# Kernel tuning notes

Measured on AMD Instinct MI355X. Metric: run time of the kernel, lower is better.

The kernel has to match this reference:

```python
import jax, jax.numpy as jnp
import numpy as np

B, C, G = 2, 256, 32
SPATIAL = (16, 16, 16)
EPS = 1e-5


def setup_inputs() -> dict:
    key = jax.random.key(0)
    ks = jax.random.split(key, 11)
    s = 1.0 / np.sqrt(C)
    x = jax.random.normal(ks[0], (B, C) + SPATIAL, dtype=jnp.float32)
    mk = lambda k: jax.random.normal(k, (C, C), dtype=jnp.float32) * s
    return {
        "x": x,
        "Wq": mk(ks[1]), "bq": jnp.zeros((C,), jnp.float32),
        "Wk": mk(ks[2]), "bk": jnp.zeros((C,), jnp.float32),
        "Wv": mk(ks[3]), "bv": jnp.zeros((C,), jnp.float32),
        "Wo": mk(ks[4]), "bo": jnp.zeros((C,), jnp.float32),
        "gamma": jnp.ones((C,), jnp.float32),
        "beta": jnp.zeros((C,), jnp.float32),
    }


def reference(x, Wq, bq, Wk, bk, Wv, bv, Wo, bo, gamma, beta):
    b, c = x.shape[0], x.shape[1]
    xf = x.reshape(b, c, -1)  # [B, C, N]

    def proj1x1(inp, W, bias):
        return jnp.einsum('oc,bcn->bon', W, inp) + bias[None, :, None]

    q = proj1x1(xf, Wq, bq)
    k = proj1x1(xf, Wk, bk)
    v = proj1x1(xf, Wv, bv)

    # qk[b, n, m] = sum_c q[b, c, n] * k[b, c, m]   (no 1/sqrt(C) scale, as in source)
    scores = jnp.einsum('bcn,bcm->bnm', q, k)
    w = jax.nn.softmax(scores, axis=-1)
    # h[b, c, n] = sum_m v[b, c, m] * w[b, n, m]
    h = jnp.einsum('bcm,bnm->bcn', v, w)
    h = proj1x1(h, Wo, bo)

    y = xf + h  # residual

    # GroupNorm over (channels-in-group, spatial)
    yg = y.reshape(b, G, c // G, -1)
    mu = jnp.mean(yg, axis=(2, 3), keepdims=True)
    var = jnp.var(yg, axis=(2, 3), keepdims=True)
    yn = ((yg - mu) * jax.lax.rsqrt(var + EPS)).reshape(b, c, -1)
    yn = yn * gamma[None, :, None] + beta[None, :, None]

    out = yn * jax.nn.sigmoid(yn)  # SiLU
    return out.reshape(x.shape)
```

## Files before the change

### kernel.cpp

```cpp
#include <hip/hip_runtime.h>
#include <hip/hip_bf16.h>

typedef _Float16 f16;
typedef __attribute__((ext_vector_type(8))) _Float16 f16x8;
typedef __attribute__((ext_vector_type(4))) float f32x4;

#define CD 256
#define ND 4096
#define GD 32
#define KS 4
#define KVB 64
#define NIT ((ND / KS) / KVB)

__device__ __forceinline__ void gl_lds16(const f16* g, f16* l) {
    __builtin_amdgcn_global_load_lds(
        (const __attribute__((address_space(1))) unsigned int*)g,
        (__attribute__((address_space(3))) unsigned int*)l,
        16, 0, 0);
}

__global__ __launch_bounds__(256)
void k_proj_qkv(const float* __restrict__ x,
                const float* __restrict__ Wq, const float* __restrict__ bq,
                const float* __restrict__ Wk, const float* __restrict__ bk,
                const float* __restrict__ Wv, const float* __restrict__ bv,
                f16* __restrict__ Qt, f16* __restrict__ Kt, f16* __restrict__ Vb)
{
    __shared__ f16 As[64][40];
    __shared__ f16 Bs[64][40];
    __shared__ f16 Ts[64][72];

    const int t  = threadIdx.x;
    const int n0 = blockIdx.x * 64;
    const int o0 = blockIdx.y * 64;
    const int p  = blockIdx.z % 3;
    const int bb = blockIdx.z / 3;

    const float* W    = (p == 0) ? Wq : (p == 1) ? Wk : Wv;
    const float* bias = (p == 0) ? bq : (p == 1) ? bk : bv;

    const int w  = t >> 6;
    const int l  = t & 63;
    const int lr = l & 15;
    const int lg = l >> 4;
    const int wo = (w >> 1) * 32;
    const int wn = (w & 1) * 32;

    const int sl = t & 63;
    const int k8 = (t >> 6) * 8;

    f32x4 acc[2][2] = {};

    for (int ck = 0; ck < CD; ck += 32) {
        __syncthreads();
        {
            const float* s = W + (size_t)(o0 + sl) * CD + ck + k8;
            f16x8 v;
#pragma unroll
            for (int u = 0; u < 8; ++u) v[u] = (f16)s[u];
            *(f16x8*)&As[sl][k8] = v;
        }
        {
            const float* s = x + ((size_t)bb * CD + ck + k8) * ND + n0 + sl;
            f16x8 v;
#pragma unroll
            for (int u = 0; u < 8; ++u) v[u] = (f16)s[(size_t)u * ND];
            *(f16x8*)&Bs[sl][k8] = v;
        }
        __syncthreads();
        f16x8 a0 = *(const f16x8*)&As[wo + lr][lg * 8];
        f16x8 a1 = *(const f16x8*)&As[wo + 16 + lr][lg * 8];
        f16x8 b0 = *(const f16x8*)&Bs[wn + lr][lg * 8];
        f16x8 b1 = *(const f16x8*)&Bs[wn + 16 + lr][lg * 8];
        acc[0][0] = __builtin_amdgcn_mfma_f32_16x16x32_f16(a0, b0, acc[0][0], 0, 0, 0);
        acc[0][1] = __builtin_amdgcn_mfma_f32_16x16x32_f16(a0, b1, acc[0][1], 0, 0, 0);
        acc[1][0] = __builtin_amdgcn_mfma_f32_16x16x32_f16(a1, b0, acc[1][0], 0, 0, 0);
        acc[1][1] = __builtin_amdgcn_mfma_f32_16x16x32_f16(a1, b1, acc[1][1], 0, 0, 0);
    }

    if (p < 2) {
        __syncthreads();
#pragma unroll
        for (int so = 0; so < 2; ++so)
#pragma unroll
            for (int r = 0; r < 4; ++r) {
                int orow  = wo + so * 16 + lg * 4 + r;
                float bv_ = bias[o0 + orow];
#pragma unroll
                for (int sn = 0; sn < 2; ++sn)
                    Ts[orow][wn + sn * 16 + lr] = (f16)(acc[so][sn][r] + bv_);
            }
        __syncthreads();
        f16* dst = (p == 0) ? Qt : Kt;
        int n  = t >> 2;
        int o8 = (t & 3) * 16;
        f16 tmp[16];
#pragma unroll
        for (int u = 0; u < 16; ++u) tmp[u] = Ts[o8 + u][n];
        f16* g = dst + ((size_t)bb * ND + n0 + n) * CD + o0 + o8;
        *(f16x8*)g       = *(f16x8*)&tmp[0];
        *(f16x8*)(g + 8) = *(f16x8*)&tmp[8];
    } else {
#pragma unroll
        for (int so = 0; so < 2; ++so)
#pragma unroll
            for (int r = 0; r < 4; ++r) {
                int orow  = wo + so * 16 + lg * 4 + r;
                float bv_ = bias[o0 + orow];
#pragma unroll
                for (int sn = 0; sn < 2; ++sn) {
                    int ncol = wn + sn * 16 + lr;
                    Vb[((size_t)bb * CD + o0 + orow) * ND + n0 + ncol] =
                        (f16)(acc[so][sn][r] + bv_);
                }
            }
    }
}

__global__ __launch_bounds__(512, 2)
void k_attn(const f16* __restrict__ Qt, const f16* __restrict__ Kt,
            const f16* __restrict__ Vb, f16* __restrict__ Op,
            float* __restrict__ ml)
{
    __shared__ f16 Ks[2][64 * 256];
    __shared__ f16 Vs[2][256 * 64];
    __shared__ f16 Ps[8][16][72];

    const int t  = threadIdx.x;
    const int w  = t >> 6;
    const int l  = t & 63;
    const int lr = l & 15;
    const int lg = l >> 4;
    const int ks = blockIdx.y;
    const int bb = blockIdx.z;
    const int q0 = blockIdx.x * 128 + w * 16;

    f16x8 qf[8];
#pragma unroll
    for (int kc = 0; kc < 8; ++kc)
        qf[kc] = *(const f16x8*)(Qt + ((size_t)bb * ND + q0 + lr) * CD + kc * 32 + lg * 8);

    f32x4 oacc[16] = {};
    float row_m[4], row_l[4];
#pragma unroll
    for (int r = 0; r < 4; ++r) { row_m[r] = -3.0e38f; row_l[r] = 0.f; }

    const int kv0 = ks * (ND / KS);
    const f16* ktb = Kt + (size_t)bb * ND * CD;
    const f16* vbb = Vb + (size_t)bb * CD * ND;

    auto stage = [&](int m0, int bi) {
#pragma unroll
        for (int j = 0; j < 4; ++j) {
            int v   = (w * 4 + j) * 64 + l;
            int row = v >> 5;
            int ch  = (v & 31) ^ (row & 7);
            gl_lds16(ktb + (size_t)(m0 + row) * CD + ch * 8,
                     &Ks[bi][(w * 4 + j) * 512]);
        }
#pragma unroll
        for (int j = 0; j < 4; ++j) {
            int v = (w * 4 + j) * 64 + l;
            int c = v >> 3;
            int u = (v & 7) ^ (c & 7);
            gl_lds16(vbb + (size_t)c * ND + m0 + u * 8,
                     &Vs[bi][(w * 4 + j) * 512]);
        }
    };

    stage(kv0, 0);
    __syncthreads();

    for (int it = 0; it < NIT; ++it) {
        const int bi = it & 1;
        if (it + 1 < NIT) stage(kv0 + (it + 1) * KVB, bi ^ 1);

        f32x4 s[4] = {};
#pragma unroll
        for (int kc = 0; kc < 8; ++kc) {
#pragma unroll
            for (int sub = 0; sub < 4; ++sub) {
                int row = sub * 16 + lr;
                f16x8 kf = *(const f16x8*)&Ks[bi][row * 256 + (((kc * 4 + lg) ^ (lr & 7))) * 8];
                s[sub] = __builtin_amdgcn_mfma_f32_16x16x32_f16(qf[kc], kf, s[sub], 0, 0, 0);
            }
        }

        float scl[4];
#pragma unroll
        for (int r = 0; r < 4; ++r) {
            float v0 = s[0][r], v1 = s[1][r], v2 = s[2][r], v3 = s[3][r];
            float pm = fmaxf(fmaxf(v0, v1), fmaxf(v2, v3));
            pm = fmaxf(pm, __shfl_xor(pm, 1));
            pm = fmaxf(pm, __shfl_xor(pm, 2));
            pm = fmaxf(pm, __shfl_xor(pm, 4));
            pm = fmaxf(pm, __shfl_xor(pm, 8));
            float newm = fmaxf(row_m[r], pm);
            float sc   = __expf(row_m[r] - newm);
            float p0   = __expf(v0 - newm);
            float p1   = __expf(v1 - newm);
            float p2   = __expf(v2 - newm);
            float p3   = __expf(v3 - newm);
            float ps   = p0 + p1 + p2 + p3;
            ps += __shfl_xor(ps, 1);
            ps += __shfl_xor(ps, 2);
            ps += __shfl_xor(ps, 4);
            ps += __shfl_xor(ps, 8);
            row_l[r] = row_l[r] * sc + ps;
            row_m[r] = newm;
            scl[r]   = sc;
            int n = lg * 4 + r;
            Ps[w][n][lr]      = (f16)p0;
            Ps[w][n][16 + lr] = (f16)p1;
            Ps[w][n][32 + lr] = (f16)p2;
            Ps[w][n][48 + lr] = (f16)p3;
        }
        {
            int src  = (lr >> 2) * 16;
            float t0 = __shfl(scl[0], src);
            float t1 = __shfl(scl[1], src);
            float t2 = __shfl(scl[2], src);
            float t3 = __shfl(scl[3], src);
            int rr   = lr & 3;
            float fa = (rr & 1) ? t1 : t0;
            float fb = (rr & 1) ? t3 : t2;
            float f  = (rr & 2) ? fb : fa;
#pragma unroll
            for (int ct = 0; ct < 16; ++ct) {
                oacc[ct][0] *= f; oacc[ct][1] *= f;
                oacc[ct][2] *= f; oacc[ct][3] *= f;
            }
        }
#pragma unroll
        for (int mc = 0; mc < 2; ++mc) {
            f16x8 pf = *(const f16x8*)&Ps[w][lr][mc * 32 + lg * 8];
#pragma unroll
            for (int ct = 0; ct < 16; ++ct) {
                f16x8 vf = *(const f16x8*)&Vs[bi][(ct * 16 + lr) * 64 + (((mc * 4 + lg) ^ (lr & 7))) * 8];
                oacc[ct] = __builtin_amdgcn_mfma_f32_16x16x32_f16(vf, pf, oacc[ct], 0, 0, 0);
            }
        }
        __syncthreads();
    }

#pragma unroll
    for (int ct = 0; ct < 16; ++ct)
#pragma unroll
        for (int r = 0; r < 4; ++r) {
            int cch = ct * 16 + lg * 4 + r;
            Op[(((size_t)ks * 2 + bb) * CD + cch) * ND + q0 + lr] = (f16)oacc[ct][r];
        }
    if (lr == 0) {
#pragma unroll
        for (int r = 0; r < 4; ++r) {
            int n = q0 + lg * 4 + r;
            ml[((ks * 2 + bb) * 2 + 0) * ND + n] = row_m[r];
            ml[((ks * 2 + bb) * 2 + 1) * ND + n] = row_l[r];
        }
    }
}

__global__ __launch_bounds__(256)
void k_comb(const f16* __restrict__ Op, const float* __restrict__ ml,
            f16* __restrict__ Hb)
{
    const int t  = threadIdx.x;
    const int tn = t & 63;
    const int cg = t >> 6;
    const int n  = blockIdx.x * 64 + tn;
    const int b  = blockIdx.y;

    float m[KS], lv[KS];
#pragma unroll
    for (int ks = 0; ks < KS; ++ks) {
        m[ks]  = ml[((ks * 2 + b) * 2 + 0) * ND + n];
        lv[ks] = ml[((ks * 2 + b) * 2 + 1) * ND + n];
    }
    float M = fmaxf(fmaxf(m[0], m[1]), fmaxf(m[2], m[3]));
    float wgt[KS];
    float L = 0.f;
#pragma unroll
    for (int ks = 0; ks < KS; ++ks) { wgt[ks] = __expf(m[ks] - M); L += wgt[ks] * lv[ks]; }
    float inv = 1.0f / L;

#pragma unroll 4
    for (int i = 0; i < 64; ++i) {
        int c = cg * 64 + i;
        float acc = 0.f;
#pragma unroll
        for (int ks = 0; ks < KS; ++ks)
            acc += wgt[ks] * (float)Op[(((size_t)ks * 2 + b) * CD + c) * ND + n];
        Hb[((size_t)b * CD + c) * ND + n] = (f16)(acc * inv);
    }
}

__global__ __launch_bounds__(256)
void k_proj_o(const f16* __restrict__ Hb, const float* __restrict__ Wo,
              const float* __restrict__ bo, const float* __restrict__ x,
              float* __restrict__ Y)
{
    __shared__ f16 As[64][40];
    __shared__ f16 Bs[64][40];

    const int t  = threadIdx.x;
    const int n0 = blockIdx.x * 64;
    const int o0 = blockIdx.y * 64;
    const int bb = blockIdx.z;

    const int w  = t >> 6;
    const int l  = t & 63;
    const int lr = l & 15;
    const int lg = l >> 4;
    const int wo = (w >> 1) * 32;
    const int wn = (w & 1) * 32;

    const int sl = t & 63;
    const int k8 = (t >> 6) * 8;

    f32x4 acc[2][2] = {};

    for (int ck = 0; ck < CD; ck += 32) {
        __syncthreads();
        {
            const float* s = Wo + (size_t)(o0 + sl) * CD + ck + k8;
            f16x8 v;
#pragma unroll
            for (int u = 0; u < 8; ++u) v[u] = (f16)s[u];
            *(f16x8*)&As[sl][k8] = v;
        }
        {
            const f16* s = Hb + ((size_t)bb * CD + ck + k8) * ND + n0 + sl;
            f16x8 v;
#pragma unroll
            for (int u = 0; u < 8; ++u) v[u] = s[(size_t)u * ND];
            *(f16x8*)&Bs[sl][k8] = v;
        }
        __syncthreads();
        f16x8 a0 = *(const f16x8*)&As[wo + lr][lg * 8];
        f16x8 a1 = *(const f16x8*)&As[wo + 16 + lr][lg * 8];
        f16x8 b0 = *(const f16x8*)&Bs[wn + lr][lg * 8];
        f16x8 b1 = *(const f16x8*)&Bs[wn + 16 + lr][lg * 8];
        acc[0][0] = __builtin_amdgcn_mfma_f32_16x16x32_f16(a0, b0, acc[0][0], 0, 0, 0);
        acc[0][1] = __builtin_amdgcn_mfma_f32_16x16x32_f16(a0, b1, acc[0][1], 0, 0, 0);
        acc[1][0] = __builtin_amdgcn_mfma_f32_16x16x32_f16(a1, b0, acc[1][0], 0, 0, 0);
        acc[1][1] = __builtin_amdgcn_mfma_f32_16x16x32_f16(a1, b1, acc[1][1], 0, 0, 0);
    }

#pragma unroll
    for (int so = 0; so < 2; ++so)
#pragma unroll
        for (int r = 0; r < 4; ++r) {
            int orow  = wo + so * 16 + lg * 4 + r;
            float bv_ = bo[o0 + orow];
#pragma unroll
            for (int sn = 0; sn < 2; ++sn) {
                int ncol   = wn + sn * 16 + lr;
                size_t idx = ((size_t)bb * CD + o0 + orow) * ND + n0 + ncol;
                Y[idx] = acc[so][sn][r] + bv_ + x[idx];
            }
        }
}

__global__ __launch_bounds__(256)
void k_stats(const float* __restrict__ Y, float* __restrict__ stats)
{
    const int g = blockIdx.x, b = blockIdx.y;
    const float* base = Y + ((size_t)b * CD + g * 8) * ND;
    float s = 0.f, s2 = 0.f;
    for (int i = threadIdx.x; i < (8 * ND) / 4; i += 256) {
        float4 v = ((const float4*)base)[i];
        s  += v.x + v.y + v.z + v.w;
        s2 += v.x * v.x + v.y * v.y + v.z * v.z + v.w * v.w;
    }
#pragma unroll
    for (int m = 1; m < 64; m <<= 1) {
        s  += __shfl_xor(s, m);
        s2 += __shfl_xor(s2, m);
    }
    __shared__ float red[8];
    if ((threadIdx.x & 63) == 0) {
        red[(threadIdx.x >> 6) * 2]     = s;
        red[(threadIdx.x >> 6) * 2 + 1] = s2;
    }
    __syncthreads();
    if (threadIdx.x == 0) {
        float S  = red[0] + red[2] + red[4] + red[6];
        float S2 = red[1] + red[3] + red[5] + red[7];
        float mean = S / 32768.f;
        float var  = S2 / 32768.f - mean * mean;
        stats[(b * GD + g) * 2]     = mean;
        stats[(b * GD + g) * 2 + 1] = rsqrtf(var + 1e-5f);
    }
}

__global__ __launch_bounds__(256)
void k_norm_silu(const float* __restrict__ Y, const float* __restrict__ stats,
                 const float* __restrict__ gamma, const float* __restrict__ beta,
                 float* __restrict__ out)
{
    size_t i4 = (size_t)blockIdx.x * 256 + threadIdx.x;
    int c = (int)((i4 / (ND / 4)) % CD);
    int b = (int)(i4 / ((size_t)CD * (ND / 4)));
    float mean = stats[(b * GD + c / 8) * 2];
    float rstd = stats[(b * GD + c / 8) * 2 + 1];
    float ga = gamma[c], be = beta[c];
    float4 v = ((const float4*)Y)[i4];
    float in[4] = { v.x, v.y, v.z, v.w };
    float ob[4];
#pragma unroll
    for (int u = 0; u < 4; ++u) {
        float yn = (in[u] - mean) * rstd * ga + be;
        float sg = 1.0f / (1.0f + __expf(-yn));
        ob[u] = yn * sg;
    }
    *(float4*)(out + i4 * 4) = *(float4*)ob;
}

extern "C" void kernel_launch(void* const* d_in, const int* in_sizes, int n_in,
                              void* d_out, int out_size, void* d_ws, size_t ws_size,
                              hipStream_t stream)
{
    const float* x     = (const float*)d_in[0];
    const float* Wq    = (const float*)d_in[1];
    const float* bq    = (const float*)d_in[2];
    const float* Wk    = (const float*)d_in[3];
    const float* bk    = (const float*)d_in[4];
    const float* Wv    = (const float*)d_in[5];
    const float* bv    = (const float*)d_in[6];
    const float* Wo    = (const float*)d_in[7];
    const float* bo    = (const float*)d_in[8];
    const float* gamma = (const float*)d_in[9];
    const float* beta  = (const float*)d_in[10];

    char* ws = (char*)d_ws;
    f16*   Qt    = (f16*)(ws);
    f16*   Kt    = (f16*)(ws + (4u << 20));
    f16*   Vb    = (f16*)(ws + (8u << 20));
    f16*   Hb    = (f16*)(ws + (12u << 20));
    f16*   Op    = (f16*)(ws + (16u << 20));
    float* ml    = (float*)(ws + (32u << 20));
    float* Y     = (float*)(ws + (16u << 20));
    float* stats = (float*)(ws + (33u << 20));

    k_proj_qkv<<<dim3(64, 4, 6), 256, 0, stream>>>(x, Wq, bq, Wk, bk, Wv, bv, Qt, Kt, Vb);
    k_attn<<<dim3(32, KS, 2), 512, 0, stream>>>(Qt, Kt, Vb, Op, ml);
    k_comb<<<dim3(64, 2), 256, 0, stream>>>(Op, ml, Hb);
    k_proj_o<<<dim3(64, 4, 2), 256, 0, stream>>>(Hb, Wo, bo, x, Y);
    k_stats<<<dim3(32, 2), 256, 0, stream>>>(Y, stats);
    k_norm_silu<<<2048, 256, 0, stream>>>(Y, stats, gamma, beta, (float*)d_out);
}
```

Baseline: 126.3 us.

## Restructure flash attention: 32-query waves, KV split 8, transposed score tiles, lazy rescale

The attention kernel now uses 256-thread blocks where each wave owns 32 queries. It uses 32-wide KV tiles, computes transposed score tiles so row reductions need only cross-lane shuffles, packs P stores, skips the O rescale when the max did not change, and sets MFMA priority. The KV split factor becomes a template parameter. It is raised to 8 when the workspace is large enough, which doubles parallelism across the key dimension. The combine step is split into a small weight kernel and a vectorized 8-wide combine kernel. This adds more partial-output traffic and one extra launch in exchange for higher occupancy, better K/V reuse per LDS load and cheaper softmax bookkeeping.

```diff
diff --git a/kernel.cpp b/kernel.cpp
--- a/kernel.cpp
+++ b/kernel.cpp
@@ -2,15 +2,14 @@
 #include <hip/hip_bf16.h>
 
 typedef _Float16 f16;
+typedef __attribute__((ext_vector_type(4))) _Float16 f16x4;
 typedef __attribute__((ext_vector_type(8))) _Float16 f16x8;
 typedef __attribute__((ext_vector_type(4))) float f32x4;
 
 #define CD 256
 #define ND 4096
 #define GD 32
-#define KS 4
-#define KVB 64
-#define NIT ((ND / KS) / KVB)
+#define KVB 32
 
 __device__ __forceinline__ void gl_lds16(const f16* g, f16* l) {
     __builtin_amdgcn_global_load_lds(
@@ -117,14 +116,15 @@
     }
 }
 
-__global__ __launch_bounds__(512, 2)
+template<int KSN>
+__global__ __launch_bounds__(256, 2)
 void k_attn(const f16* __restrict__ Qt, const f16* __restrict__ Kt,
             const f16* __restrict__ Vb, f16* __restrict__ Op,
             float* __restrict__ ml)
 {
-    __shared__ f16 Ks[2][64 * 256];
-    __shared__ f16 Vs[2][256 * 64];
-    __shared__ f16 Ps[8][16][72];
+    __shared__ f16 Ks[2][32 * 256];
+    __shared__ f16 Vs[2][256 * 32];
+    __shared__ f16 Pl[4][32][40];
 
     const int t  = threadIdx.x;
     const int w  = t >> 6;
@@ -133,165 +133,185 @@
     const int lg = l >> 4;
     const int ks = blockIdx.y;
     const int bb = blockIdx.z;
-    const int q0 = blockIdx.x * 128 + w * 16;
-
-    f16x8 qf[8];
-#pragma unroll
-    for (int kc = 0; kc < 8; ++kc)
-        qf[kc] = *(const f16x8*)(Qt + ((size_t)bb * ND + q0 + lr) * CD + kc * 32 + lg * 8);
-
-    f32x4 oacc[16] = {};
-    float row_m[4], row_l[4];
-#pragma unroll
-    for (int r = 0; r < 4; ++r) { row_m[r] = -3.0e38f; row_l[r] = 0.f; }
-
-    const int kv0 = ks * (ND / KS);
+    const int q0 = blockIdx.x * 128 + w * 32;
+
+    f16x8 qf[2][8];
+#pragma unroll
+    for (int qs = 0; qs < 2; ++qs)
+#pragma unroll
+        for (int kc = 0; kc < 8; ++kc)
+            qf[qs][kc] = *(const f16x8*)(Qt + ((size_t)bb * ND + q0 + qs * 16 + lr) * CD + kc * 32 + lg * 8);
+
+    f32x4 oacc[2][16] = {};
+    float row_m[2] = { -3.0e38f, -3.0e38f };
+    float row_l[2] = { 0.f, 0.f };
+
+    const int kv0 = ks * (ND / KSN);
     const f16* ktb = Kt + (size_t)bb * ND * CD;
     const f16* vbb = Vb + (size_t)bb * CD * ND;
 
+    int koff[4], voff[4];
+#pragma unroll
+    for (int j = 0; j < 4; ++j) {
+        int v   = (w * 4 + j) * 64 + l;
+        int row = v >> 5;
+        int ch  = (v & 31) ^ (row & 7);
+        koff[j] = row * CD + ch * 8;
+        int c   = v >> 2;
+        int u   = (v & 3) ^ ((c >> 1) & 3);
+        voff[j] = c * ND + u * 8;
+    }
+
     auto stage = [&](int m0, int bi) {
 #pragma unroll
-        for (int j = 0; j < 4; ++j) {
-            int v   = (w * 4 + j) * 64 + l;
-            int row = v >> 5;
-            int ch  = (v & 31) ^ (row & 7);
-            gl_lds16(ktb + (size_t)(m0 + row) * CD + ch * 8,
-                     &Ks[bi][(w * 4 + j) * 512]);
-        }
-#pragma unroll
-        for (int j = 0; j < 4; ++j) {
-            int v = (w * 4 + j) * 64 + l;
-            int c = v >> 3;
-            int u = (v & 7) ^ (c & 7);
-            gl_lds16(vbb + (size_t)c * ND + m0 + u * 8,
-                     &Vs[bi][(w * 4 + j) * 512]);
-        }
+        for (int j = 0; j < 4; ++j)
+            gl_lds16(ktb + (size_t)m0 * CD + koff[j], &Ks[bi][(w * 4 + j) * 512]);
+#pragma unroll
+        for (int j = 0; j < 4; ++j)
+            gl_lds16(vbb + m0 + voff[j], &Vs[bi][(w * 4 + j) * 512]);
     };
 
     stage(kv0, 0);
     __syncthreads();
 
+    const int NIT = (ND / KSN) / KVB;
     for (int it = 0; it < NIT; ++it) {
         const int bi = it & 1;
         if (it + 1 < NIT) stage(kv0 + (it + 1) * KVB, bi ^ 1);
 
-        f32x4 s[4] = {};
+        f32x4 s[2][2] = {};
+        __builtin_amdgcn_s_setprio(1);
 #pragma unroll
         for (int kc = 0; kc < 8; ++kc) {
-#pragma unroll
-            for (int sub = 0; sub < 4; ++sub) {
-                int row = sub * 16 + lr;
-                f16x8 kf = *(const f16x8*)&Ks[bi][row * 256 + (((kc * 4 + lg) ^ (lr & 7))) * 8];
-                s[sub] = __builtin_amdgcn_mfma_f32_16x16x32_f16(qf[kc], kf, s[sub], 0, 0, 0);
+            int chs = ((kc * 4 + lg) ^ (lr & 7)) * 8;
+            f16x8 k0 = *(const f16x8*)&Ks[bi][(lr) * 256 + chs];
+            f16x8 k1 = *(const f16x8*)&Ks[bi][(16 + lr) * 256 + chs];
+            s[0][0] = __builtin_amdgcn_mfma_f32_16x16x32_f16(k0, qf[0][kc], s[0][0], 0, 0, 0);
+            s[1][0] = __builtin_amdgcn_mfma_f32_16x16x32_f16(k1, qf[0][kc], s[1][0], 0, 0, 0);
+            s[0][1] = __builtin_amdgcn_mfma_f32_16x16x32_f16(k0, qf[1][kc], s[0][1], 0, 0, 0);
+            s[1][1] = __builtin_amdgcn_mfma_f32_16x16x32_f16(k1, qf[1][kc], s[1][1], 0, 0, 0);
+        }
+        __builtin_amdgcn_s_setprio(0);
+
+#pragma unroll
+        for (int qs = 0; qs < 2; ++qs) {
+            float pm = fmaxf(
+                fmaxf(fmaxf(s[0][qs][0], s[0][qs][1]), fmaxf(s[0][qs][2], s[0][qs][3])),
+                fmaxf(fmaxf(s[1][qs][0], s[1][qs][1]), fmaxf(s[1][qs][2], s[1][qs][3])));
+            pm = fmaxf(pm, __shfl_xor(pm, 16));
+            pm = fmaxf(pm, __shfl_xor(pm, 32));
+            float nm = fmaxf(row_m[qs], pm);
+            float sc = __expf(row_m[qs] - nm);
+            float p0 = __expf(s[0][qs][0] - nm);
+            float p1 = __expf(s[0][qs][1] - nm);
+            float p2 = __expf(s[0][qs][2] - nm);
+            float p3 = __expf(s[0][qs][3] - nm);
+            float p4 = __expf(s[1][qs][0] - nm);
+            float p5 = __expf(s[1][qs][1] - nm);
+            float p6 = __expf(s[1][qs][2] - nm);
+            float p7 = __expf(s[1][qs][3] - nm);
+            float ps = ((p0 + p1) + (p2 + p3)) + ((p4 + p5) + (p6 + p7));
+            ps += __shfl_xor(ps, 16);
+            ps += __shfl_xor(ps, 32);
+            bool chg = nm > row_m[qs];
+            row_l[qs] = row_l[qs] * sc + ps;
+            row_m[qs] = nm;
+            if (__any(chg)) {
+#pragma unroll
+                for (int ct = 0; ct < 16; ++ct) {
+                    oacc[qs][ct][0] *= sc; oacc[qs][ct][1] *= sc;
+                    oacc[qs][ct][2] *= sc; oacc[qs][ct][3] *= sc;
+                }
             }
-        }
-
-        float scl[4];
-#pragma unroll
-        for (int r = 0; r < 4; ++r) {
-            float v0 = s[0][r], v1 = s[1][r], v2 = s[2][r], v3 = s[3][r];
-            float pm = fmaxf(fmaxf(v0, v1), fmaxf(v2, v3));
-            pm = fmaxf(pm, __shfl_xor(pm, 1));
-            pm = fmaxf(pm, __shfl_xor(pm, 2));
-            pm = fmaxf(pm, __shfl_xor(pm, 4));
-            pm = fmaxf(pm, __shfl_xor(pm, 8));
-            float newm = fmaxf(row_m[r], pm);
-            float sc   = __expf(row_m[r] - newm);
-            float p0   = __expf(v0 - newm);
-            float p1   = __expf(v1 - newm);
-            float p2   = __expf(v2 - newm);
-            float p3   = __expf(v3 - newm);
-            float ps   = p0 + p1 + p2 + p3;
-            ps += __shfl_xor(ps, 1);
-            ps += __shfl_xor(ps, 2);
-            ps += __shfl_xor(ps, 4);
-            ps += __shfl_xor(ps, 8);
-            row_l[r] = row_l[r] * sc + ps;
-            row_m[r] = newm;
-            scl[r]   = sc;
-            int n = lg * 4 + r;
-            Ps[w][n][lr]      = (f16)p0;
-            Ps[w][n][16 + lr] = (f16)p1;
-            Ps[w][n][32 + lr] = (f16)p2;
-            Ps[w][n][48 + lr] = (f16)p3;
-        }
-        {
-            int src  = (lr >> 2) * 16;
-            float t0 = __shfl(scl[0], src);
-            float t1 = __shfl(scl[1], src);
-            float t2 = __shfl(scl[2], src);
-            float t3 = __shfl(scl[3], src);
-            int rr   = lr & 3;
-            float fa = (rr & 1) ? t1 : t0;
-            float fb = (rr & 1) ? t3 : t2;
-            float f  = (rr & 2) ? fb : fa;
-#pragma unroll
-            for (int ct = 0; ct < 16; ++ct) {
-                oacc[ct][0] *= f; oacc[ct][1] *= f;
-                oacc[ct][2] *= f; oacc[ct][3] *= f;
+            f16x4 pk0 = { (f16)p0, (f16)p1, (f16)p2, (f16)p3 };
+            f16x4 pk1 = { (f16)p4, (f16)p5, (f16)p6, (f16)p7 };
+            *(f16x4*)&Pl[w][qs * 16 + lr][lg * 4]      = pk0;
+            *(f16x4*)&Pl[w][qs * 16 + lr][16 + lg * 4] = pk1;
+        }
+
+        f16x8 pf0 = *(const f16x8*)&Pl[w][lr][lg * 8];
+        f16x8 pf1 = *(const f16x8*)&Pl[w][16 + lr][lg * 8];
+        __builtin_amdgcn_s_setprio(1);
+#pragma unroll
+        for (int ct = 0; ct < 16; ++ct) {
+            f16x8 vf = *(const f16x8*)&Vs[bi][(ct * 16 + lr) * 32 + ((lg ^ ((lr >> 1) & 3))) * 8];
+            oacc[0][ct] = __builtin_amdgcn_mfma_f32_16x16x32_f16(vf, pf0, oacc[0][ct], 0, 0, 0);
+            oacc[1][ct] = __builtin_amdgcn_mfma_f32_16x16x32_f16(vf, pf1, oacc[1][ct], 0, 0, 0);
+        }
+        __builtin_amdgcn_s_setprio(0);
+        __syncthreads();
+    }
+
+#pragma unroll
+    for (int qs = 0; qs < 2; ++qs)
+#pragma unroll
+        for (int ct = 0; ct < 16; ++ct)
+#pragma unroll
+            for (int r = 0; r < 4; ++r) {
+                int cch = ct * 16 + lg * 4 + r;
+                Op[(((size_t)ks * 2 + bb) * CD + cch) * ND + q0 + qs * 16 + lr] =
+                    (f16)oacc[qs][ct][r];
             }
-        }
-#pragma unroll
-        for (int mc = 0; mc < 2; ++mc) {
-            f16x8 pf = *(const f16x8*)&Ps[w][lr][mc * 32 + lg * 8];
-#pragma unroll
-            for (int ct = 0; ct < 16; ++ct) {
-                f16x8 vf = *(const f16x8*)&Vs[bi][(ct * 16 + lr) * 64 + (((mc * 4 + lg) ^ (lr & 7))) * 8];
-                oacc[ct] = __builtin_amdgcn_mfma_f32_16x16x32_f16(vf, pf, oacc[ct], 0, 0, 0);
-            }
-        }
-        __syncthreads();
-    }
-
-#pragma unroll
-    for (int ct = 0; ct < 16; ++ct)
-#pragma unroll
-        for (int r = 0; r < 4; ++r) {
-            int cch = ct * 16 + lg * 4 + r;
-            Op[(((size_t)ks * 2 + bb) * CD + cch) * ND + q0 + lr] = (f16)oacc[ct][r];
-        }
-    if (lr == 0) {
-#pragma unroll
-        for (int r = 0; r < 4; ++r) {
-            int n = q0 + lg * 4 + r;
-            ml[((ks * 2 + bb) * 2 + 0) * ND + n] = row_m[r];
-            ml[((ks * 2 + bb) * 2 + 1) * ND + n] = row_l[r];
-        }
-    }
-}
-
-__global__ __launch_bounds__(256)
-void k_comb(const f16* __restrict__ Op, const float* __restrict__ ml,
-            f16* __restrict__ Hb)
-{
-    const int t  = threadIdx.x;
-    const int tn = t & 63;
-    const int cg = t >> 6;
-    const int n  = blockIdx.x * 64 + tn;
-    const int b  = blockIdx.y;
-
-    float m[KS], lv[KS];
-#pragma unroll
-    for (int ks = 0; ks < KS; ++ks) {
+    if (lg == 0) {
+#pragma unroll
+        for (int qs = 0; qs < 2; ++qs) {
+            int n = q0 + qs * 16 + lr;
+            ml[((ks * 2 + bb) * 2 + 0) * ND + n] = row_m[qs];
+            ml[((ks * 2 + bb) * 2 + 1) * ND + n] = row_l[qs];
+        }
+    }
+}
+
+template<int KSN>
+__global__ __launch_bounds__(256)
+void k_ml(const float* __restrict__ ml, float* __restrict__ wq)
+{
+    int i = blockIdx.x * 256 + threadIdx.x;
+    int b = i / ND, n = i % ND;
+    float m[KSN], lv[KSN];
+#pragma unroll
+    for (int ks = 0; ks < KSN; ++ks) {
         m[ks]  = ml[((ks * 2 + b) * 2 + 0) * ND + n];
         lv[ks] = ml[((ks * 2 + b) * 2 + 1) * ND + n];
     }
-    float M = fmaxf(fmaxf(m[0], m[1]), fmaxf(m[2], m[3]));
-    float wgt[KS];
-    float L = 0.f;
-#pragma unroll
-    for (int ks = 0; ks < KS; ++ks) { wgt[ks] = __expf(m[ks] - M); L += wgt[ks] * lv[ks]; }
+    float M = m[0];
+#pragma unroll
+    for (int ks = 1; ks < KSN; ++ks) M = fmaxf(M, m[ks]);
+    float wgt[KSN], L = 0.f;
+#pragma unroll
+    for (int ks = 0; ks < KSN; ++ks) { wgt[ks] = __expf(m[ks] - M); L += wgt[ks] * lv[ks]; }
     float inv = 1.0f / L;
-
-#pragma unroll 4
-    for (int i = 0; i < 64; ++i) {
-        int c = cg * 64 + i;
-        float acc = 0.f;
-#pragma unroll
-        for (int ks = 0; ks < KS; ++ks)
-            acc += wgt[ks] * (float)Op[(((size_t)ks * 2 + b) * CD + c) * ND + n];
-        Hb[((size_t)b * CD + c) * ND + n] = (f16)(acc * inv);
-    }
+#pragma unroll
+    for (int ks = 0; ks < KSN; ++ks)
+        wq[(ks * 2 + b) * ND + n] = wgt[ks] * inv;
+}
+
+template<int KSN>
+__global__ __launch_bounds__(256)
+void k_comb(const f16* __restrict__ Op, const float* __restrict__ wq,
+            f16* __restrict__ Hb)
+{
+    size_t i = (size_t)blockIdx.x * 256 + threadIdx.x;
+    int n0 = (int)(i % (ND / 8)) * 8;
+    int c  = (int)((i / (ND / 8)) % CD);
+    int b  = (int)(i / ((size_t)CD * (ND / 8)));
+
+    float acc[8] = {};
+#pragma unroll
+    for (int ks = 0; ks < KSN; ++ks) {
+        f16x8 o = *(const f16x8*)(Op + (((size_t)ks * 2 + b) * CD + c) * ND + n0);
+        const float* wp = wq + (ks * 2 + b) * ND + n0;
+        float4 w0 = *(const float4*)wp;
+        float4 w1 = *(const float4*)(wp + 4);
+        acc[0] += w0.x * (float)o[0]; acc[1] += w0.y * (float)o[1];
+        acc[2] += w0.z * (float)o[2]; acc[3] += w0.w * (float)o[3];
+        acc[4] += w1.x * (float)o[4]; acc[5] += w1.y * (float)o[5];
+        acc[6] += w1.z * (float)o[6]; acc[7] += w1.w * (float)o[7];
+    }
+    f16x8 h;
+#pragma unroll
+    for (int u = 0; u < 8; ++u) h[u] = (f16)acc[u];
+    *(f16x8*)(Hb + ((size_t)b * CD + c) * ND + n0) = h;
 }
 
 __global__ __launch_bounds__(256)
@@ -433,19 +453,38 @@
     const float* beta  = (const float*)d_in[10];
 
     char* ws = (char*)d_ws;
-    f16*   Qt    = (f16*)(ws);
-    f16*   Kt    = (f16*)(ws + (4u << 20));
-    f16*   Vb    = (f16*)(ws + (8u << 20));
-    f16*   Hb    = (f16*)(ws + (12u << 20));
-    f16*   Op    = (f16*)(ws + (16u << 20));
-    float* ml    = (float*)(ws + (32u << 20));
-    float* Y     = (float*)(ws + (16u << 20));
-    float* stats = (float*)(ws + (33u << 20));
+    f16* Qt = (f16*)(ws);
+    f16* Kt = (f16*)(ws + (4u << 20));
+    f16* Vb = (f16*)(ws + (8u << 20));
+    f16* Hb = (f16*)(ws + (12u << 20));
+    f16* Op = (f16*)(ws + (16u << 20));
+    float* Y = (float*)(ws + (16u << 20));
+
+    const bool big = ws_size >= (50ull << 20);
 
     k_proj_qkv<<<dim3(64, 4, 6), 256, 0, stream>>>(x, Wq, bq, Wk, bk, Wv, bv, Qt, Kt, Vb);
-    k_attn<<<dim3(32, KS, 2), 512, 0, stream>>>(Qt, Kt, Vb, Op, ml);
-    k_comb<<<dim3(64, 2), 256, 0, stream>>>(Op, ml, Hb);
-    k_proj_o<<<dim3(64, 4, 2), 256, 0, stream>>>(Hb, Wo, bo, x, Y);
-    k_stats<<<dim3(32, 2), 256, 0, stream>>>(Y, stats);
-    k_norm_silu<<<2048, 256, 0, stream>>>(Y, stats, gamma, beta, (float*)d_out);
-}
+
+    if (big) {
+        constexpr int KSN = 8;
+        float* ml    = (float*)(ws + (48u << 20));
+        float* wq    = (float*)(ws + (48u << 20) + (768u << 10));
+        float* stats = (float*)(ws + (49u << 20) + (512u << 10));
+        k_attn<KSN><<<dim3(32, KSN, 2), 256, 0, stream>>>(Qt, Kt, Vb, Op, ml);
+        k_ml<KSN><<<dim3((2 * ND) / 256), 256, 0, stream>>>(ml, wq);
+        k_comb<KSN><<<dim3((2 * CD * ND / 8) / 256), 256, 0, stream>>>(Op, wq, Hb);
+        k_proj_o<<<dim3(64, 4, 2), 256, 0, stream>>>(Hb, Wo, bo, x, Y);
+        k_stats<<<dim3(32, 2), 256, 0, stream>>>(Y, stats);
+        k_norm_silu<<<2048, 256, 0, stream>>>(Y, stats, gamma, beta, (float*)d_out);
+    } else {
+        constexpr int KSN = 4;
+        float* ml    = (float*)(ws + (32u << 20));
+        float* wq    = (float*)(ws + (32u << 20) + (512u << 10));
+        float* stats = (float*)(ws + (33u << 20));
+        k_attn<KSN><<<dim3(32, KSN, 2), 256, 0, stream>>>(Qt, Kt, Vb, Op, ml);
+        k_ml<KSN><<<dim3((2 * ND) / 256), 256, 0, stream>>>(ml, wq);
+        k_comb<KSN><<<dim3((2 * CD * ND / 8) / 256), 256, 0, stream>>>(Op, wq, Hb);
+        k_proj_o<<<dim3(64, 4, 2), 256, 0, stream>>>(Hb, Wo, bo, x, Y);
+        k_stats<<<dim3(32, 2), 256, 0, stream>>>(Y, stats);
+        k_norm_silu<<<2048, 256, 0, stream>>>(Y, stats, gamma, beta, (float*)d_out);
+    }
+}
```

After: 121.3 us. 4.0% less time.
